# Kernel tuning notes

Measured on AMD Instinct MI355X. Metric: run time of the kernel, lower is better.

The kernel has to match this reference:

```python
import jax, jax.numpy as jnp
import numpy as np

B, IDIM, ODIM, MSIZE = 8192, 4096, 4096, 128
ICOUNT = (IDIM + MSIZE - 1) // MSIZE        # 32
MCOUNT = (max(IDIM, ODIM) + MSIZE - 1) // MSIZE  # 32
OCOUNT = (ODIM + MSIZE - 1) // MSIZE        # 32


def setup_inputs() -> dict:
    key = jax.random.key(0)
    ks = jax.random.split(key, 7)
    s_in = 1.0 / np.sqrt(ICOUNT)
    s_m = 1.0 / np.sqrt(MSIZE)
    s_out = 1.0 / np.sqrt(MCOUNT)
    return {
        "x": jax.random.normal(ks[0], (B, IDIM), dtype=jnp.float32),
        "W_in": jax.random.normal(ks[1], (MCOUNT, ICOUNT), dtype=jnp.float32) * s_in,
        "b_in": jax.random.normal(ks[2], (MCOUNT,), dtype=jnp.float32) * s_in,
        "W_mods": jax.random.normal(ks[3], (MCOUNT, MSIZE, MSIZE), dtype=jnp.float32) * s_m,
        "b_mods": jax.random.normal(ks[4], (MCOUNT, MSIZE), dtype=jnp.float32) * s_m,
        "W_out": jax.random.normal(ks[5], (OCOUNT, MCOUNT), dtype=jnp.float32) * s_out,
        "b_out": jax.random.normal(ks[6], (OCOUNT,), dtype=jnp.float32) * s_out,
        "odim": ODIM,
    }


def reference(x, W_in, b_in, W_mods, b_mods, W_out, b_out, odim):
    msize = W_mods.shape[-1]
    b = x.shape[0]
    idim = x.shape[-1]
    rem = idim % msize  # static
    if rem != 0:
        x = jnp.pad(x, ((0, 0), (0, msize - rem)))
    icount = x.shape[-1] // msize
    # reshape to blocks then tail_permute (swap last two axes)
    x = x.reshape(b, icount, msize).swapaxes(-1, -2)      # [B, msize, icount]
    x = jnp.einsum('bmi,ci->bmc', x, W_in) + b_in          # fcin -> [B, msize, mcount]
    x = x.swapaxes(-1, -2)                                 # [B, mcount, msize]
    # per-block submodule: Linear(msize->msize) per block, vectorized over blocks
    x = jnp.einsum('bcm,cnm->bcn', x, W_mods) + b_mods     # [B, mcount, msize]
    x = x.swapaxes(-1, -2)                                 # [B, msize, mcount]
    x = jnp.einsum('bmc,oc->bmo', x, W_out) + b_out        # fcout -> [B, msize, ocount]
    x = x.reshape(b, -1)[:, :odim]                         # [B, odim]
    return x  # act = Identity
```

## Files before the change

kernel.cpp:

```cpp
#include <hip/hip_runtime.h>
#include <stdint.h>


#define BT    16
#define NTHR  1024
#define GRID  512
#define IDIM  4096
#define ODIM  4096

typedef __attribute__((ext_vector_type(8))) __bf16 bf16x8;
typedef __attribute__((ext_vector_type(4))) float  floatx4;

union BF8 { uint32_t w[4]; unsigned short h[8]; bf16x8 v; };

__device__ __forceinline__ unsigned short f2bf(float f) {
    return __builtin_bit_cast(unsigned short, (__bf16)f);
}

#define YP_BT 136
#define YP_C  2184
#define WP_BT 36
#define WP_N  584
#define WCH_HALF (16 * WP_N)

__device__ __forceinline__ void bar_lgkm() {
    asm volatile("s_waitcnt lgkmcnt(0)" ::: "memory");
    __builtin_amdgcn_s_barrier();
    __builtin_amdgcn_sched_barrier(0);
}

template<bool WBF16>
__global__ __launch_bounds__(NTHR, 4)
void tinymod_fused(const float* __restrict__ x,
                   const float* __restrict__ W_in,
                   const float* __restrict__ b_in,
                   const void*  __restrict__ wmods,
                   const float* __restrict__ b_mods,
                   const float* __restrict__ W_out,
                   const float* __restrict__ b_out,
                   float* __restrict__ out)
{
    __shared__ unsigned short ylds[32 * YP_C] __attribute__((aligned(16)));
    unsigned short* const wch = ylds;

    const int tid  = threadIdx.x;
    const int lane = tid & 63;
    const int wave = tid >> 6;
    const int l15  = lane & 15;
    const int grp  = lane >> 4;
    const int row0 = blockIdx.x * BT;

    const float bin0 = b_in[l15],  bin1 = b_in[16 + l15];
    const float bo0  = b_out[l15], bo1  = b_out[16 + l15];
    BF8 winf[2], woutf[2];
    #pragma unroll
    for (int cc = 0; cc < 2; cc++) {
        const float* p = W_in  + (l15 + 16*cc) * 32 + grp * 8;
        const float* q = W_out + (l15 + 16*cc) * 32 + grp * 8;
        #pragma unroll
        for (int j = 0; j < 8; j++) { winf[cc].h[j] = f2bf(p[j]); woutf[cc].h[j] = f2bf(q[j]); }
    }

    const float* xb = x + (row0 + wave) * IDIM + l15;
    float xr[8];
    #pragma unroll
    for (int j = 0; j < 8; j++) xr[j] = xb[(grp*8 + j) * 128];

    for (int mb = 0; mb < 8; mb++) {
        float xn[8];
        if (mb < 7) {
            #pragma unroll
            for (int j = 0; j < 8; j++) xn[j] = xb[(grp*8 + j) * 128 + (mb + 1) * 16];
        }
        BF8 a;
        #pragma unroll
        for (int j = 0; j < 8; j++) a.h[j] = f2bf(xr[j]);
        #pragma unroll
        for (int cc = 0; cc < 2; cc++) {
            floatx4 acc = {0.f, 0.f, 0.f, 0.f};
            acc = __builtin_amdgcn_mfma_f32_16x16x32_bf16(a.v, winf[cc].v, acc, 0, 0, 0);
            const float bi = cc ? bin1 : bin0;
            unsigned short h[4];
            #pragma unroll
            for (int r = 0; r < 4; r++) h[r] = f2bf(acc[r] + bi);
            uint2 pk;
            pk.x = (uint32_t)h[0] | ((uint32_t)h[1] << 16);
            pk.y = (uint32_t)h[2] | ((uint32_t)h[3] << 16);
            *(uint2*)&ylds[(l15 + 16*cc)*YP_C + wave*YP_BT + mb*16 + grp*4] = pk;
        }
        if (mb < 7) {
            #pragma unroll
            for (int j = 0; j < 8; j++) xr[j] = xn[j];
        }
    }
    bar_lgkm();

    BF8 af[2][4];
    #pragma unroll
    for (int ci = 0; ci < 2; ci++) {
        const int c = 2*wave + ci;
        #pragma unroll
        for (int kc = 0; kc < 4; kc++) {
            const uint4 v = *(const uint4*)&ylds[c*YP_C + l15*YP_BT + kc*32 + grp*8];
            af[ci][kc].w[0] = v.x; af[ci][kc].w[1] = v.y;
            af[ci][kc].w[2] = v.z; af[ci][kc].w[3] = v.w;
        }
    }
    bar_lgkm();

    const unsigned short* __restrict__ wm16 = (const unsigned short*)wmods;
    const float*          __restrict__ wm32 = (const float*)wmods;

    for (int nb = 0; nb < 8; nb++) {
        unsigned short* const wchb = wch + (nb & 1) * WCH_HALF;

        float bm[2];
        BF8 b[2][4];
        #pragma unroll
        for (int ci = 0; ci < 2; ci++) {
            const int c = 2*wave + ci;
            bm[ci] = b_mods[c*128 + nb*16 + l15];
            #pragma unroll
            for (int kc = 0; kc < 4; kc++) {
                const int wbase = (c*128 + nb*16 + l15)*128 + kc*32 + grp*8;
                if (WBF16) {
                    const uint4 bv = *(const uint4*)&wm16[wbase];
                    b[ci][kc].w[0] = bv.x; b[ci][kc].w[1] = bv.y;
                    b[ci][kc].w[2] = bv.z; b[ci][kc].w[3] = bv.w;
                } else {
                    const float* wp = wm32 + wbase;
                    #pragma unroll
                    for (int j = 0; j < 8; j++) b[ci][kc].h[j] = f2bf(wp[j]);
                }
            }
        }
        floatx4 acc[2];
        #pragma unroll
        for (int ci = 0; ci < 2; ci++) {
            floatx4 s = {0.f, 0.f, 0.f, 0.f};
            #pragma unroll
            for (int kc = 0; kc < 4; kc++)
                s = __builtin_amdgcn_mfma_f32_16x16x32_bf16(af[ci][kc].v, b[ci][kc].v, s, 0, 0, 0);
            acc[ci] = s;
        }
        #pragma unroll
        for (int r = 0; r < 4; r++) {
            const unsigned short h0 = f2bf(acc[0][r] + bm[0]);
            const unsigned short h1 = f2bf(acc[1][r] + bm[1]);
            const uint32_t pk = (uint32_t)h0 | ((uint32_t)h1 << 16);
            *(uint32_t*)&wchb[l15*WP_N + (grp*4 + r)*WP_BT + 2*wave] = pk;
        }
        bar_lgkm();

        BF8 a3;
        {
            const int off = wave*WP_N + l15*WP_BT + grp*8;
            const uint2 u0 = *(const uint2*)&wchb[off];
            const uint2 u1 = *(const uint2*)&wchb[off + 4];
            a3.w[0] = u0.x; a3.w[1] = u0.y; a3.w[2] = u1.x; a3.w[3] = u1.y;
        }
        #pragma unroll
        for (int oc = 0; oc < 2; oc++) {
            floatx4 v = {0.f, 0.f, 0.f, 0.f};
            v = __builtin_amdgcn_mfma_f32_16x16x32_bf16(a3.v, woutf[oc].v, v, 0, 0, 0);
            const float bo = oc ? bo1 : bo0;
            float* po = out + row0*ODIM + (nb*16 + wave)*32 + oc*16 + l15;
            #pragma unroll
            for (int r = 0; r < 4; r++) {
                const int bt = grp*4 + r;
                po[bt*ODIM] = v[r] + bo;
            }
        }
    }
}

__global__ void wmods_to_bf16(const float* __restrict__ w, unsigned short* __restrict__ o) {
    const int i = (blockIdx.x * 256 + threadIdx.x) * 4;
    const float4 f = *(const float4*)(w + i);
    uint2 pk;
    pk.x = (uint32_t)f2bf(f.x) | ((uint32_t)f2bf(f.y) << 16);
    pk.y = (uint32_t)f2bf(f.z) | ((uint32_t)f2bf(f.w) << 16);
    *(uint2*)(o + i) = pk;
}

extern "C" void kernel_launch(void* const* d_in, const int* in_sizes, int n_in,
                              void* d_out, int out_size, void* d_ws, size_t ws_size,
                              hipStream_t stream)
{
    const float* x     = (const float*)d_in[0];
    const float* W_in  = (const float*)d_in[1];
    const float* b_in  = (const float*)d_in[2];
    const float* Wm    = (const float*)d_in[3];
    const float* b_m   = (const float*)d_in[4];
    const float* W_out = (const float*)d_in[5];
    const float* b_out = (const float*)d_in[6];
    float* out = (float*)d_out;

    const size_t wm_elems = 32u * 128u * 128u;
    if (ws_size >= wm_elems * sizeof(unsigned short)) {
        unsigned short* wbf = (unsigned short*)d_ws;
        wmods_to_bf16<<<(int)(wm_elems / (256 * 4)), 256, 0, stream>>>(Wm, wbf);
        tinymod_fused<true><<<GRID, NTHR, 0, stream>>>(x, W_in, b_in, (const void*)wbf,
                                                       b_m, W_out, b_out, out);
    } else {
        tinymod_fused<false><<<GRID, NTHR, 0, stream>>>(x, W_in, b_in, (const void*)Wm,
                                                        b_m, W_out, b_out, out);
    }
}
```

Measured before the change: 305.0 us.

## Coalesce x loads via LDS staging and stage output tiles for vectorized stores

The x input is now read with contiguous float4 loads across full rows, converted to bf16 and transposed through a new LDS buffer, with a three-deep register prefetch. This replaces the strided per-lane scalar gathers. Outputs of the final MFMA stage are staged in LDS and written back as contiguous float4 row segments instead of scattered scalar stores. The cost is extra barriers per stage, more LDS use (which may reduce occupancy), and a fully unrolled nb loop.

```diff
diff --git a/kernel.cpp b/kernel.cpp
--- a/kernel.cpp
+++ b/kernel.cpp
@@ -21,12 +21,13 @@
 #define YP_C  2184
 #define WP_BT 36
 #define WP_N  584
-#define WCH_HALF (16 * WP_N)
+#define WCH_ELE (16 * WP_N)
+#define OB_P  516
 
 __device__ __forceinline__ void bar_lgkm() {
     asm volatile("s_waitcnt lgkmcnt(0)" ::: "memory");
     __builtin_amdgcn_s_barrier();
-    __builtin_amdgcn_sched_barrier(0);
+    asm volatile("" ::: "memory");
 }
 
 template<bool WBF16>
@@ -41,7 +42,9 @@
                    float* __restrict__ out)
 {
     __shared__ unsigned short ylds[32 * YP_C] __attribute__((aligned(16)));
-    unsigned short* const wch = ylds;
+    __shared__ unsigned short xbuf[8192]      __attribute__((aligned(16)));
+    unsigned short* const wch  = ylds;
+    float* const obuf = (float*)((char*)ylds + 4 * WCH_ELE);
 
     const int tid  = threadIdx.x;
     const int lane = tid & 63;
@@ -61,20 +64,43 @@
         for (int j = 0; j < 8; j++) { winf[cc].h[j] = f2bf(p[j]); woutf[cc].h[j] = f2bf(q[j]); }
     }
 
-    const float* xb = x + (row0 + wave) * IDIM + l15;
-    float xr[8];
-    #pragma unroll
-    for (int j = 0; j < 8; j++) xr[j] = xb[(grp*8 + j) * 128];
-
-    for (int mb = 0; mb < 8; mb++) {
-        float xn[8];
-        if (mb < 7) {
-            #pragma unroll
-            for (int j = 0; j < 8; j++) xn[j] = xb[(grp*8 + j) * 128 + (mb + 1) * 16];
-        }
+    const int bt2 = tid >> 9;
+    const int C0  = (tid & 511) * 8;
+    const int xw  = ((bt2*8 + ((C0 >> 4) & 7))*32 + (C0 >> 7))*16 + (C0 & 15);
+    const int bt2w = wave >> 3;
+    const int mbw  = wave & 7;
+    const int fb   = ((bt2w*8 + mbw)*32 + grp*8)*16 + l15;
+
+    float xr[3][8];
+    #pragma unroll
+    for (int p = 0; p < 3; p++) {
+        const float* ptr = x + (row0 + 2*p + bt2)*IDIM + C0;
+        const float4 f0 = *(const float4*)ptr;
+        const float4 f1 = *(const float4*)(ptr + 4);
+        xr[p][0]=f0.x; xr[p][1]=f0.y; xr[p][2]=f0.z; xr[p][3]=f0.w;
+        xr[p][4]=f1.x; xr[p][5]=f1.y; xr[p][6]=f1.z; xr[p][7]=f1.w;
+    }
+
+    #pragma unroll
+    for (int cb = 0; cb < 8; cb++) {
+        const int s = cb % 3;
+        BF8 t;
+        #pragma unroll
+        for (int j = 0; j < 8; j++) t.h[j] = f2bf(xr[s][j]);
+        uint4 val; val.x = t.w[0]; val.y = t.w[1]; val.z = t.w[2]; val.w = t.w[3];
+        *(uint4*)&xbuf[xw] = val;
+        if (cb + 3 < 8) {
+            const float* ptr = x + (row0 + 2*(cb+3) + bt2)*IDIM + C0;
+            const float4 f0 = *(const float4*)ptr;
+            const float4 f1 = *(const float4*)(ptr + 4);
+            xr[s][0]=f0.x; xr[s][1]=f0.y; xr[s][2]=f0.z; xr[s][3]=f0.w;
+            xr[s][4]=f1.x; xr[s][5]=f1.y; xr[s][6]=f1.z; xr[s][7]=f1.w;
+        }
+        bar_lgkm();
+
         BF8 a;
         #pragma unroll
-        for (int j = 0; j < 8; j++) a.h[j] = f2bf(xr[j]);
+        for (int j = 0; j < 8; j++) a.h[j] = xbuf[fb + j*16];
         #pragma unroll
         for (int cc = 0; cc < 2; cc++) {
             floatx4 acc = {0.f, 0.f, 0.f, 0.f};
@@ -86,14 +112,10 @@
             uint2 pk;
             pk.x = (uint32_t)h[0] | ((uint32_t)h[1] << 16);
             pk.y = (uint32_t)h[2] | ((uint32_t)h[3] << 16);
-            *(uint2*)&ylds[(l15 + 16*cc)*YP_C + wave*YP_BT + mb*16 + grp*4] = pk;
-        }
-        if (mb < 7) {
-            #pragma unroll
-            for (int j = 0; j < 8; j++) xr[j] = xn[j];
-        }
-    }
-    bar_lgkm();
+            *(uint2*)&ylds[(l15 + 16*cc)*YP_C + (2*cb + bt2w)*YP_BT + mbw*16 + grp*4] = pk;
+        }
+        bar_lgkm();
+    }
 
     BF8 af[2][4];
     #pragma unroll
@@ -111,8 +133,9 @@
     const unsigned short* __restrict__ wm16 = (const unsigned short*)wmods;
     const float*          __restrict__ wm32 = (const float*)wmods;
 
+    #pragma unroll
     for (int nb = 0; nb < 8; nb++) {
-        unsigned short* const wchb = wch + (nb & 1) * WCH_HALF;
+        unsigned short* const wchb = wch + (nb & 1) * WCH_ELE;
 
         float bm[2];
         BF8 b[2][4];
@@ -164,12 +187,19 @@
             floatx4 v = {0.f, 0.f, 0.f, 0.f};
             v = __builtin_amdgcn_mfma_f32_16x16x32_bf16(a3.v, woutf[oc].v, v, 0, 0, 0);
             const float bo = oc ? bo1 : bo0;
-            float* po = out + row0*ODIM + (nb*16 + wave)*32 + oc*16 + l15;
-            #pragma unroll
-            for (int r = 0; r < 4; r++) {
-                const int bt = grp*4 + r;
-                po[bt*ODIM] = v[r] + bo;
-            }
+            #pragma unroll
+            for (int r = 0; r < 4; r++)
+                obuf[(grp*4 + r)*OB_P + wave*32 + oc*16 + l15] = v[r] + bo;
+        }
+        bar_lgkm();
+
+        {
+            const int ec = (tid & 63) * 8;
+            const float4 o0 = *(const float4*)&obuf[wave*OB_P + ec];
+            const float4 o1 = *(const float4*)&obuf[wave*OB_P + ec + 4];
+            float* po = out + (row0 + wave)*ODIM + nb*512 + ec;
+            *(float4*)po       = o0;
+            *(float4*)(po + 4) = o1;
         }
     }
 }
```

Result: slower. 313.2 us (+2.7%).
